# Kernel tuning notes

Measured on AMD Instinct MI355X. Metric: run time of the kernel, lower is better.

## Reference

```python
import jax, jax.numpy as jnp
import numpy as np

VOCAB, EMB, HID, LAYERS, SEQ, BATCH = 128, 512, 1024, 2, 256, 64


def _lstm_layer(xs, h0, c0, Wih, Whh, b):
    # xs: [S, B, in], h0/c0: [B, H], Wih: [4H, in], Whh: [4H, H], b: [4H]
    def step(carry, x_t):
        h, c = carry
        gates = x_t @ Wih.T + h @ Whh.T + b  # [B, 4H]
        i, f, g, o = jnp.split(gates, 4, axis=-1)
        c = jax.nn.sigmoid(f) * c + jax.nn.sigmoid(i) * jnp.tanh(g)
        h = jax.nn.sigmoid(o) * jnp.tanh(c)
        return (h, c), h

    (h, c), ys = jax.lax.scan(step, (h0, c0), xs)
    return ys, h, c


def setup_inputs() -> dict:
    key = jax.random.key(0)
    ks = jax.random.split(key, 10)
    s = 0.05
    inp = {
        "x": jax.random.randint(ks[0], (SEQ, BATCH), 0, VOCAB),
        "h0": jnp.zeros((LAYERS, BATCH, HID), jnp.float32),
        "c0": jnp.zeros((LAYERS, BATCH, HID), jnp.float32),
        "emb": jax.random.normal(ks[1], (VOCAB, EMB), jnp.float32) * s,
        "Wih0": jax.random.normal(ks[2], (4 * HID, EMB), jnp.float32) * s,
        "Whh0": jax.random.normal(ks[3], (4 * HID, HID), jnp.float32) * s,
        "b0": jnp.zeros((4 * HID,), jnp.float32),
        "Wih1": jax.random.normal(ks[4], (4 * HID, HID), jnp.float32) * s,
        "Whh1": jax.random.normal(ks[5], (4 * HID, HID), jnp.float32) * s,
        "b1": jnp.zeros((4 * HID,), jnp.float32),
        "Wfc": jax.random.normal(ks[6], (VOCAB, HID), jnp.float32) * s,
        "bfc": jnp.zeros((VOCAB,), jnp.float32),
    }
    return inp


def reference(x, h0, c0, emb, Wih0, Whh0, b0, Wih1, Whh1, b1, Wfc, bfc):
    xs = emb[x]  # [S, B, EMB] embedding lookup
    ys0, h_0, c_0 = _lstm_layer(xs, h0[0], c0[0], Wih0, Whh0, b0)
    ys1, h_1, c_1 = _lstm_layer(ys0, h0[1], c0[1], Wih1, Whh1, b1)
    last = ys1[-1]  # [B, HID]
    logits = last @ Wfc.T + bfc  # [B, VOCAB]
    hidden = (jnp.stack([h_0, h_1]), jnp.stack([c_0, c_1]))
    return (logits, hidden)
```

## Files before the change

### kernel.cpp

```cpp
#include <hip/hip_runtime.h>
#include <hip/hip_bf16.h>

#define SEQ   256
#define BATCH 64
#define HID   1024
#define EMBD  512
#define VOCAB 128
#define G4    4096
#define HBS   (BATCH * HID)

typedef short bf16x8_t __attribute__((ext_vector_type(8)));
typedef float f32x4_t  __attribute__((ext_vector_type(4)));
using bf16 = __hip_bfloat16;

__device__ __forceinline__ float sigm(float v) { return 1.f / (1.f + expf(-v)); }

__device__ __forceinline__ void cstore4(void* p, unsigned d) {
    asm volatile("global_store_dword %0, %1, off sc0 sc1" :: "v"(p), "v"(d) : "memory");
}

__global__ void cast_f32_bf16(const float* __restrict__ src, bf16* __restrict__ dst, int n) {
    int i = blockIdx.x * blockDim.x + threadIdx.x;
    int stride = gridDim.x * blockDim.x;
    for (; i < n; i += stride) dst[i] = __float2bfloat16(src[i]);
}

__global__ void init_all(const float* __restrict__ h0,
                         bf16* __restrict__ r0, bf16* __restrict__ r1,
                         unsigned* __restrict__ flags) {
    int i = blockIdx.x * blockDim.x + threadIdx.x;
    if (i < 512) flags[i] = 0u;
    int stride = gridDim.x * blockDim.x;
    for (int k = i; k < HBS; k += stride) {
        r0[k] = __float2bfloat16(h0[k]);
        r1[k] = __float2bfloat16(h0[HBS + k]);
    }
}

__global__ __launch_bounds__(256) void emb_gemm(
    const bf16* __restrict__ emb_bf, const bf16* __restrict__ Wih0_bf,
    const float* __restrict__ b0, float* __restrict__ E) {
    __shared__ float pb[4 * 128 * 17];
    const int tid = threadIdx.x, l = tid & 63, w = tid >> 6;
    const int lm = l & 15, k8 = (l >> 4) << 3;
    const int colbase = blockIdx.x * 16;
    const int gcol = colbase + lm;
    const int kq = w * 128;

    f32x4_t acc[8];
    #pragma unroll
    for (int rt = 0; rt < 8; ++rt) acc[rt] = f32x4_t{0.f, 0.f, 0.f, 0.f};
    bf16x8_t bf[4];
    #pragma unroll
    for (int k = 0; k < 4; ++k)
        bf[k] = *reinterpret_cast<const bf16x8_t*>(Wih0_bf + gcol * EMBD + kq + k * 32 + k8);
    #pragma unroll
    for (int k = 0; k < 4; ++k)
        #pragma unroll
        for (int rt = 0; rt < 8; ++rt) {
            bf16x8_t a = *reinterpret_cast<const bf16x8_t*>(
                emb_bf + (rt * 16 + lm) * EMBD + kq + k * 32 + k8);
            acc[rt] = __builtin_amdgcn_mfma_f32_16x16x32_bf16(a, bf[k], acc[rt], 0, 0, 0);
        }
    const int r0 = (l >> 4) << 2;
    #pragma unroll
    for (int rt = 0; rt < 8; ++rt)
        #pragma unroll
        for (int r = 0; r < 4; ++r)
            pb[(w * 128 + rt * 16 + r0 + r) * 17 + lm] = acc[rt][r];
    __syncthreads();
    #pragma unroll
    for (int i = 0; i < 8; ++i) {
        int p = tid + i * 256;
        int m = p >> 4, cc = p & 15;
        float g = pb[(0 * 128 + m) * 17 + cc] + pb[(1 * 128 + m) * 17 + cc]
                + pb[(2 * 128 + m) * 17 + cc] + pb[(3 * 128 + m) * 17 + cc];
        E[m * G4 + colbase + cc] = g + b0[colbase + cc];
    }
}

__device__ __forceinline__ void stage_slice(const char* slotB, char* Aregion,
                                            int kByte, int l) {
    #pragma unroll
    for (int i = 0; i < 32; ++i) {
        const int ci  = i * 64 + l;
        const int row = ci >> 5, kb = ci & 31;
        const char* g = slotB + row * 2048 + kByte + ((kb ^ (row & 7)) << 4);
        __builtin_amdgcn_global_load_lds(
            (const __attribute__((address_space(1))) unsigned*)g,
            (__attribute__((address_space(3))) unsigned*)(Aregion + i * 1024),
            16, 0, 0);
    }
}

__device__ __forceinline__ void issue_w(bf16x8_t (&bw)[2][8], const bf16* W,
                                        int gcol0, int gcol1, int kg, int lk) {
    #pragma unroll
    for (int nt = 0; nt < 2; ++nt) {
        const bf16* wb = W + (size_t)(nt == 0 ? gcol0 : gcol1) * HID + kg * 256 + lk * 8;
        #pragma unroll
        for (int kc = 0; kc < 8; ++kc)
            bw[nt][kc] = *reinterpret_cast<const bf16x8_t*>(wb + kc * 32);
    }
}

__device__ __forceinline__ void gemm_compute(const char* Aregion,
                                             const bf16x8_t (&bw)[2][8],
                                             int lm, int lk, f32x4_t (&acc)[4][2]) {
    asm volatile("s_waitcnt vmcnt(0)" ::: "memory");
    __builtin_amdgcn_sched_barrier(0);
    #pragma unroll
    for (int kc = 0; kc < 8; ++kc) {
        bf16x8_t a[4];
        #pragma unroll
        for (int mt = 0; mt < 4; ++mt) {
            const int row = mt * 16 + lm;
            a[mt] = *reinterpret_cast<const bf16x8_t*>(
                Aregion + row * 512 + ((kc * 64 + lk * 16) ^ ((row & 7) << 4)));
        }
        #pragma unroll
        for (int mt = 0; mt < 4; ++mt) {
            acc[mt][0] = __builtin_amdgcn_mfma_f32_16x16x32_bf16(a[mt], bw[0][kc], acc[mt][0], 0, 0, 0);
            acc[mt][1] = __builtin_amdgcn_mfma_f32_16x16x32_bf16(a[mt], bw[1][kc], acc[mt][1], 0, 0, 0);
        }
    }
}

__device__ __forceinline__ void pollslice(const unsigned* fbase, int kg,
                                          unsigned target, int l) {
    const unsigned* fp = fbase + kg * 32 + (l & 31);
    bool ok = (__hip_atomic_load(fp, __ATOMIC_RELAXED,
                                 __HIP_MEMORY_SCOPE_AGENT) >= target);
    while (!__all((int)ok)) {
        __builtin_amdgcn_s_sleep(1);
        ok = (__hip_atomic_load(fp, __ATOMIC_RELAXED,
                                __HIP_MEMORY_SCOPE_AGENT) >= target);
    }
}

template<int GRP>
__device__ __forceinline__ void run_layer(
    const int* __restrict__ x,
    const bf16* __restrict__ Wx, const bf16* __restrict__ Wh,
    const float* __restrict__ E, const float* __restrict__ b1,
    const float* __restrict__ c0,
    bf16* __restrict__ rSelf, const bf16* __restrict__ rOther,
    unsigned* __restrict__ flags, float* __restrict__ out,
    char* __restrict__ Abuf, float* __restrict__ pbuf, int tid, int wg)
{
    const int gl = wg & 127;
    const int hb = gl * 8;
    const int l  = tid & 63, kg = tid >> 6;
    const int lm = l & 15, lk = l >> 4;
    char* Areg = Abuf + kg * 32768;
    const int kByte = kg * 512;

    const int gcol0 = (0 + (lm >> 3)) * HID + hb + (lm & 7);
    const int gcol1 = (2 + (lm >> 3)) * HID + hb + (lm & 7);

    const int am = tid >> 2, cp = tid & 3;
    const int cc0 = cp * 2, col0 = hb + cc0;
    float creg[2];
    creg[0] = c0[GRP * HBS + am * HID + col0];
    creg[1] = c0[GRP * HBS + am * HID + col0 + 1];

    const unsigned* fA = flags;
    const unsigned* fOwn = flags + GRP * 128;
    unsigned* fMine = (unsigned*)(fOwn + gl);

    const int s_begin = (GRP == 0) ? 0 : 1;
    const int s_end   = (GRP == 0) ? SEQ : SEQ + 1;

    f32x4_t acc[4][2];
    auto zacc = [&]() {
        #pragma unroll
        for (int mt = 0; mt < 4; ++mt) {
            acc[mt][0] = f32x4_t{0.f, 0.f, 0.f, 0.f};
            acc[mt][1] = f32x4_t{0.f, 0.f, 0.f, 0.f};
        }
    };

    if (GRP == 1) {
        zacc();
        bf16x8_t bwx[2][8];
        issue_w(bwx, Wx, gcol0, gcol1, kg, lk);
        pollslice(fA, kg, 1u, l);
        stage_slice((const char*)(rOther + (size_t)1 * HBS), Areg, kByte, l);
        gemm_compute(Areg, bwx, lm, lk, acc);
        asm volatile("s_waitcnt lgkmcnt(0)" ::: "memory");
        __builtin_amdgcn_sched_barrier(0);
    }

    for (int s = s_begin; s < s_end; ++s) {
        float ep[4][2];
        if (GRP == 0) {
            const int xv = x[s * BATCH + am];
            const float* Ep = E + (size_t)xv * G4 + col0;
            #pragma unroll
            for (int sec = 0; sec < 4; ++sec) {
                ep[sec][0] = Ep[sec * HID];
                ep[sec][1] = Ep[sec * HID + 1];
            }
            zacc();
        }

        {
            bf16x8_t bw[2][8];
            issue_w(bw, Wh, gcol0, gcol1, kg, lk);
            if (GRP == 0) {
                pollslice(fOwn, kg, (unsigned)s, l);
                stage_slice((const char*)(rSelf + (size_t)s * HBS), Areg, kByte, l);
            } else {
                pollslice(fOwn, kg, (unsigned)(s - 1), l);
                stage_slice((const char*)(rSelf + (size_t)(s - 1) * HBS), Areg, kByte, l);
            }
            gemm_compute(Areg, bw, lm, lk, acc);
        }

        if (kg < 2) {
            #pragma unroll
            for (int mt = 0; mt < 4; ++mt)
                #pragma unroll
                for (int nt = 0; nt < 2; ++nt)
                    #pragma unroll
                    for (int r = 0; r < 4; ++r)
                        pbuf[(kg * 64 + mt * 16 + lk * 4 + r) * 34 + nt * 16 + lm]
                            = acc[mt][nt][r];
        }
        __syncthreads();
        if (kg >= 2) {
            #pragma unroll
            for (int mt = 0; mt < 4; ++mt)
                #pragma unroll
                for (int nt = 0; nt < 2; ++nt)
                    #pragma unroll
                    for (int r = 0; r < 4; ++r) {
                        float* p = &pbuf[((kg - 2) * 64 + mt * 16 + lk * 4 + r) * 34
                                         + nt * 16 + lm];
                        *p += acc[mt][nt][r];
                    }
        }
        __syncthreads();

        float g[4][2];
        #pragma unroll
        for (int sec = 0; sec < 4; ++sec) {
            const float* p0 = &pbuf[(0 * 64 + am) * 34 + sec * 8 + cc0];
            const float* p1 = &pbuf[(1 * 64 + am) * 34 + sec * 8 + cc0];
            g[sec][0] = p0[0] + p1[0];
            g[sec][1] = p0[1] + p1[1];
        }
        if (GRP == 0) {
            #pragma unroll
            for (int sec = 0; sec < 4; ++sec) {
                g[sec][0] += ep[sec][0];
                g[sec][1] += ep[sec][1];
            }
        } else {
            #pragma unroll
            for (int sec = 0; sec < 4; ++sec) {
                g[sec][0] += b1[sec * HID + col0];
                g[sec][1] += b1[sec * HID + col0 + 1];
            }
        }

        float hn[2];
        #pragma unroll
        for (int j = 0; j < 2; ++j) {
            float si = sigm(g[0][j]);
            float sf = sigm(g[1][j]);
            float tg = tanhf(g[2][j]);
            float so = sigm(g[3][j]);
            float cn = sf * creg[j] + si * tg;
            hn[j] = so * tanhf(cn);
            creg[j] = cn;
        }
        unsigned short u0 = __builtin_bit_cast(unsigned short, __float2bfloat16(hn[0]));
        unsigned short u1 = __builtin_bit_cast(unsigned short, __float2bfloat16(hn[1]));
        const int wslot = (GRP == 0) ? s + 1 : s;
        cstore4(rSelf + (size_t)wslot * HBS + am * HID + col0,
                (unsigned)u0 | ((unsigned)u1 << 16));

        const bool last = (GRP == 0) ? (s == SEQ - 1) : (s == SEQ);
        if (last) {
            float* oh = out + BATCH * VOCAB + GRP * HBS;
            float* oc = out + BATCH * VOCAB + 2 * HBS + GRP * HBS;
            oh[am * HID + col0]     = hn[0];
            oh[am * HID + col0 + 1] = hn[1];
            oc[am * HID + col0]     = creg[0];
            oc[am * HID + col0 + 1] = creg[1];
        }

        asm volatile("s_waitcnt vmcnt(0)" ::: "memory");
        __syncthreads();
        if (tid == 0) cstore4(fMine, (unsigned)wslot);

        if (GRP == 1 && s + 1 < s_end) {
            zacc();
            bf16x8_t bwx[2][8];
            issue_w(bwx, Wx, gcol0, gcol1, kg, lk);
            pollslice(fA, kg, (unsigned)(s + 1), l);
            stage_slice((const char*)(rOther + (size_t)(s + 1) * HBS), Areg, kByte, l);
            gemm_compute(Areg, bwx, lm, lk, acc);
            asm volatile("s_waitcnt lgkmcnt(0)" ::: "memory");
            __builtin_amdgcn_sched_barrier(0);
        }
    }
}

__global__ __launch_bounds__(256, 1) void lstm_persist(
    const int* __restrict__ x,
    const bf16* __restrict__ Whh0, const bf16* __restrict__ Wih1,
    const bf16* __restrict__ Whh1,
    const float* __restrict__ E, const float* __restrict__ b1,
    const float* __restrict__ c0,
    bf16* __restrict__ r0, bf16* __restrict__ r1,
    unsigned* __restrict__ flags, float* __restrict__ out)
{
    __shared__ char lds[131072 + 2 * 64 * 34 * 4];
    char*  Abuf = lds;
    float* pbuf = (float*)(lds + 131072);
    const int tid = threadIdx.x, wg = blockIdx.x;
    if (wg < 128)
        run_layer<0>(x, nullptr, Whh0, E, nullptr, c0, r0, nullptr, flags, out,
                     Abuf, pbuf, tid, wg);
    else
        run_layer<1>(x, Wih1, Whh1, E, b1, c0, r1, r0, flags, out,
                     Abuf, pbuf, tid, wg);
}

__global__ void logits_kernel(const float* __restrict__ h, const float* __restrict__ Wfc,
                              const float* __restrict__ bfc, float* __restrict__ out) {
    int t = blockIdx.x * blockDim.x + threadIdx.x;
    if (t >= BATCH * VOCAB) return;
    int m = t >> 7, v = t & 127;
    const float4* hp = reinterpret_cast<const float4*>(h + (size_t)m * HID);
    const float4* wp = reinterpret_cast<const float4*>(Wfc + (size_t)v * HID);
    float acc = 0.f;
    #pragma unroll 4
    for (int k = 0; k < HID / 4; ++k) {
        float4 a = hp[k], w = wp[k];
        acc += a.x * w.x + a.y * w.y + a.z * w.z + a.w * w.w;
    }
    out[t] = acc + bfc[v];
}

extern "C" void kernel_launch(void* const* d_in, const int* in_sizes, int n_in,
                              void* d_out, int out_size, void* d_ws, size_t ws_size,
                              hipStream_t stream) {
    const int*   x    = (const int*)d_in[0];
    const float* h0   = (const float*)d_in[1];
    const float* c0   = (const float*)d_in[2];
    const float* emb  = (const float*)d_in[3];
    const float* Wih0 = (const float*)d_in[4];
    const float* Whh0 = (const float*)d_in[5];
    const float* b0   = (const float*)d_in[6];
    const float* Wih1 = (const float*)d_in[7];
    const float* Whh1 = (const float*)d_in[8];
    const float* b1   = (const float*)d_in[9];
    const float* Wfc  = (const float*)d_in[10];
    const float* bfc  = (const float*)d_in[11];
    float* out = (float*)d_out;

    char* ws = (char*)d_ws;
    size_t off = 0;
    auto alloc = [&](size_t bytes) -> void* {
        void* p = ws + off;
        off += (bytes + 255) & ~(size_t)255;
        return p;
    };
    bf16*  Whh0_bf = (bf16*)alloc((size_t)G4 * HID * 2);
    bf16*  Wih1_bf = (bf16*)alloc((size_t)G4 * HID * 2);
    bf16*  Whh1_bf = (bf16*)alloc((size_t)G4 * HID * 2);
    float* E       = (float*)alloc((size_t)VOCAB * G4 * 4);
    bf16*  r0      = (bf16*)alloc((size_t)(SEQ + 1) * HBS * 2);
    bf16*  r1      = (bf16*)alloc((size_t)(SEQ + 1) * HBS * 2);
    unsigned* flags = (unsigned*)alloc(512 * 4);
    bf16* Wih0_bf  = (bf16*)alloc((size_t)G4 * EMBD * 2);
    bf16* emb_bf   = (bf16*)alloc((size_t)VOCAB * EMBD * 2);
    (void)ws_size; (void)in_sizes; (void)n_in; (void)out_size;

    cast_f32_bf16<<<64,  256, 0, stream>>>(emb,  emb_bf,  VOCAB * EMBD);
    cast_f32_bf16<<<512, 256, 0, stream>>>(Wih0, Wih0_bf, G4 * EMBD);
    cast_f32_bf16<<<512, 256, 0, stream>>>(Whh0, Whh0_bf, G4 * HID);
    cast_f32_bf16<<<512, 256, 0, stream>>>(Wih1, Wih1_bf, G4 * HID);
    cast_f32_bf16<<<512, 256, 0, stream>>>(Whh1, Whh1_bf, G4 * HID);
    init_all<<<64, 256, 0, stream>>>(h0, r0, r1, flags);
    emb_gemm<<<G4 / 16, 256, 0, stream>>>(emb_bf, Wih0_bf, b0, E);

    lstm_persist<<<256, 256, 0, stream>>>(x, Whh0_bf, Wih1_bf, Whh1_bf,
                                          E, b1, c0, r0, r1, flags, out);

    logits_kernel<<<(BATCH * VOCAB + 255) / 256, 256, 0, stream>>>(
        out + BATCH * VOCAB + HBS, Wfc, bfc, out);
}
```

Baseline: 1.900 ms.

## Keep LSTM weight slices resident in LDS with per-wave batch split and flags

Each persistent workgroup now loads its 32-column weight slice (both Wih1 and Whh1 for layer 1) into LDS once, instead of re-reading weights from global memory every timestep. Each wave now owns 16 batch rows over the full K dimension and reads the hidden-state rows directly into registers. This removes the cross-wave partial-sum reduction through LDS and the block-wide barriers. Synchronisation moves to per-wave flags, so each wave polls only the producers for its own batch rows. In exchange it uses many registers for A fragments and serialises the full-K MFMA chain within each wave.

```diff
diff --git a/kernel.cpp b/kernel.cpp
--- a/kernel.cpp
+++ b/kernel.cpp
@@ -15,6 +15,9 @@
 
 __device__ __forceinline__ float sigm(float v) { return 1.f / (1.f + expf(-v)); }
 
+__device__ __forceinline__ void cstore2(void* p, unsigned short d) {
+    asm volatile("global_store_short %0, %1, off sc0 sc1" :: "v"(p), "v"(d) : "memory");
+}
 __device__ __forceinline__ void cstore4(void* p, unsigned d) {
     asm volatile("global_store_dword %0, %1, off sc0 sc1" :: "v"(p), "v"(d) : "memory");
 }
@@ -29,7 +32,7 @@
                          bf16* __restrict__ r0, bf16* __restrict__ r1,
                          unsigned* __restrict__ flags) {
     int i = blockIdx.x * blockDim.x + threadIdx.x;
-    if (i < 512) flags[i] = 0u;
+    if (i < 1024) flags[i] = 0u;
     int stride = gridDim.x * blockDim.x;
     for (int k = i; k < HBS; k += stride) {
         r0[k] = __float2bfloat16(h0[k]);
@@ -79,62 +82,36 @@
     }
 }
 
-__device__ __forceinline__ void stage_slice(const char* slotB, char* Aregion,
-                                            int kByte, int l) {
-    #pragma unroll
-    for (int i = 0; i < 32; ++i) {
-        const int ci  = i * 64 + l;
-        const int row = ci >> 5, kb = ci & 31;
-        const char* g = slotB + row * 2048 + kByte + ((kb ^ (row & 7)) << 4);
-        __builtin_amdgcn_global_load_lds(
-            (const __attribute__((address_space(1))) unsigned*)g,
-            (__attribute__((address_space(3))) unsigned*)(Aregion + i * 1024),
-            16, 0, 0);
-    }
-}
-
-__device__ __forceinline__ void issue_w(bf16x8_t (&bw)[2][8], const bf16* W,
-                                        int gcol0, int gcol1, int kg, int lk) {
-    #pragma unroll
-    for (int nt = 0; nt < 2; ++nt) {
-        const bf16* wb = W + (size_t)(nt == 0 ? gcol0 : gcol1) * HID + kg * 256 + lk * 8;
-        #pragma unroll
-        for (int kc = 0; kc < 8; ++kc)
-            bw[nt][kc] = *reinterpret_cast<const bf16x8_t*>(wb + kc * 32);
-    }
-}
-
-__device__ __forceinline__ void gemm_compute(const char* Aregion,
-                                             const bf16x8_t (&bw)[2][8],
-                                             int lm, int lk, f32x4_t (&acc)[4][2]) {
+__device__ __forceinline__ void pollwave(const unsigned* fbase, unsigned target, int l) {
+    const unsigned* p0 = fbase + (l & 63);
+    const unsigned* p1 = fbase + 64 + (l & 63);
+    bool ok = (__hip_atomic_load(p0, __ATOMIC_RELAXED, __HIP_MEMORY_SCOPE_AGENT) >= target)
+           && (__hip_atomic_load(p1, __ATOMIC_RELAXED, __HIP_MEMORY_SCOPE_AGENT) >= target);
+    while (!__all((int)ok)) {
+        __builtin_amdgcn_s_sleep(1);
+        ok = (__hip_atomic_load(p0, __ATOMIC_RELAXED, __HIP_MEMORY_SCOPE_AGENT) >= target)
+          && (__hip_atomic_load(p1, __ATOMIC_RELAXED, __HIP_MEMORY_SCOPE_AGENT) >= target);
+    }
+}
+
+__device__ __forceinline__ void load_av(const bf16* arow, bf16x8_t (&av)[32]) {
+    #pragma unroll
+    for (int kc = 0; kc < 32; ++kc)
+        av[kc] = *reinterpret_cast<const bf16x8_t*>(arow + kc * 32);
     asm volatile("s_waitcnt vmcnt(0)" ::: "memory");
     __builtin_amdgcn_sched_barrier(0);
-    #pragma unroll
-    for (int kc = 0; kc < 8; ++kc) {
-        bf16x8_t a[4];
-        #pragma unroll
-        for (int mt = 0; mt < 4; ++mt) {
-            const int row = mt * 16 + lm;
-            a[mt] = *reinterpret_cast<const bf16x8_t*>(
-                Aregion + row * 512 + ((kc * 64 + lk * 16) ^ ((row & 7) << 4)));
-        }
-        #pragma unroll
-        for (int mt = 0; mt < 4; ++mt) {
-            acc[mt][0] = __builtin_amdgcn_mfma_f32_16x16x32_bf16(a[mt], bw[0][kc], acc[mt][0], 0, 0, 0);
-            acc[mt][1] = __builtin_amdgcn_mfma_f32_16x16x32_bf16(a[mt], bw[1][kc], acc[mt][1], 0, 0, 0);
-        }
-    }
-}
-
-__device__ __forceinline__ void pollslice(const unsigned* fbase, int kg,
-                                          unsigned target, int l) {
-    const unsigned* fp = fbase + kg * 32 + (l & 31);
-    bool ok = (__hip_atomic_load(fp, __ATOMIC_RELAXED,
-                                 __HIP_MEMORY_SCOPE_AGENT) >= target);
-    while (!__all((int)ok)) {
-        __builtin_amdgcn_s_sleep(1);
-        ok = (__hip_atomic_load(fp, __ATOMIC_RELAXED,
-                                __HIP_MEMORY_SCOPE_AGENT) >= target);
+}
+
+__device__ __forceinline__ void gemm_m16(const char* Wbase, const bf16x8_t (&av)[32],
+                                         int lm, int lk, f32x4_t (&acc)[2]) {
+    const int swz = (lm & 7) << 4;
+    #pragma unroll
+    for (int kc = 0; kc < 32; ++kc) {
+        const int kb = (kc * 64 + lk * 16) ^ swz;
+        bf16x8_t b0 = *reinterpret_cast<const bf16x8_t*>(Wbase + lm * 2048 + kb);
+        bf16x8_t b1 = *reinterpret_cast<const bf16x8_t*>(Wbase + (16 + lm) * 2048 + kb);
+        acc[0] = __builtin_amdgcn_mfma_f32_16x16x32_bf16(av[kc], b0, acc[0], 0, 0, 0);
+        acc[1] = __builtin_amdgcn_mfma_f32_16x16x32_bf16(av[kc], b1, acc[1], 0, 0, 0);
     }
 }
 
@@ -146,162 +123,139 @@
     const float* __restrict__ c0,
     bf16* __restrict__ rSelf, const bf16* __restrict__ rOther,
     unsigned* __restrict__ flags, float* __restrict__ out,
-    char* __restrict__ Abuf, float* __restrict__ pbuf, int tid, int wg)
+    char* __restrict__ Wlds, int tid, int wg)
 {
     const int gl = wg & 127;
     const int hb = gl * 8;
-    const int l  = tid & 63, kg = tid >> 6;
+    const int l  = tid & 63, w = tid >> 6;
     const int lm = l & 15, lk = l >> 4;
-    char* Areg = Abuf + kg * 32768;
-    const int kByte = kg * 512;
-
-    const int gcol0 = (0 + (lm >> 3)) * HID + hb + (lm & 7);
-    const int gcol1 = (2 + (lm >> 3)) * HID + hb + (lm & 7);
-
-    const int am = tid >> 2, cp = tid & 3;
-    const int cc0 = cp * 2, col0 = hb + cc0;
-    float creg[2];
-    creg[0] = c0[GRP * HBS + am * HID + col0];
-    creg[1] = c0[GRP * HBS + am * HID + col0 + 1];
-
-    const unsigned* fA = flags;
-    const unsigned* fOwn = flags + GRP * 128;
-    unsigned* fMine = (unsigned*)(fOwn + gl);
+
+    {
+        const bf16* wsrc0 = (GRP == 0) ? Wh : Wx;
+        #pragma unroll 4
+        for (int i = 0; i < 16; ++i) {
+            int chunk = tid + i * 256;
+            int row = chunk >> 7, cb = chunk & 127;
+            int gc = (row >> 3) * HID + hb + (row & 7);
+            bf16x8_t v = *reinterpret_cast<const bf16x8_t*>(wsrc0 + (size_t)gc * HID + cb * 8);
+            *reinterpret_cast<bf16x8_t*>(Wlds + row * 2048 + ((cb * 16) ^ ((row & 7) << 4))) = v;
+        }
+        if (GRP == 1) {
+            #pragma unroll 4
+            for (int i = 0; i < 16; ++i) {
+                int chunk = tid + i * 256;
+                int row = chunk >> 7, cb = chunk & 127;
+                int gc = (row >> 3) * HID + hb + (row & 7);
+                bf16x8_t v = *reinterpret_cast<const bf16x8_t*>(Wh + (size_t)gc * HID + cb * 8);
+                *reinterpret_cast<bf16x8_t*>(Wlds + 65536 + row * 2048 + ((cb * 16) ^ ((row & 7) << 4))) = v;
+            }
+        }
+    }
+    __syncthreads();
+
+    const char* Wx_lds = Wlds;
+    const char* Wh_lds = (GRP == 0) ? Wlds : (Wlds + 65536);
+
+    const int col = hb + (lm & 7);
+    const int mrow0 = w * 16 + lk * 4;
+    float creg[4];
+    if (lm < 8) {
+        #pragma unroll
+        for (int r = 0; r < 4; ++r)
+            creg[r] = c0[GRP * HBS + (size_t)(mrow0 + r) * HID + col];
+    }
+    float bias[4];
+    if (GRP == 1 && lm < 8) {
+        #pragma unroll
+        for (int sec = 0; sec < 4; ++sec) bias[sec] = b1[sec * HID + col];
+    }
+
+    const unsigned* fA   = flags + w * 128;
+    const unsigned* fOwn = flags + GRP * 512 + w * 128;
+    unsigned* fMine = (unsigned*)(flags + GRP * 512 + w * 128 + gl);
 
     const int s_begin = (GRP == 0) ? 0 : 1;
     const int s_end   = (GRP == 0) ? SEQ : SEQ + 1;
 
-    f32x4_t acc[4][2];
+    f32x4_t acc[2];
     auto zacc = [&]() {
-        #pragma unroll
-        for (int mt = 0; mt < 4; ++mt) {
-            acc[mt][0] = f32x4_t{0.f, 0.f, 0.f, 0.f};
-            acc[mt][1] = f32x4_t{0.f, 0.f, 0.f, 0.f};
-        }
+        acc[0] = f32x4_t{0.f, 0.f, 0.f, 0.f};
+        acc[1] = f32x4_t{0.f, 0.f, 0.f, 0.f};
     };
+
+    bf16x8_t av[32];
 
     if (GRP == 1) {
         zacc();
-        bf16x8_t bwx[2][8];
-        issue_w(bwx, Wx, gcol0, gcol1, kg, lk);
-        pollslice(fA, kg, 1u, l);
-        stage_slice((const char*)(rOther + (size_t)1 * HBS), Areg, kByte, l);
-        gemm_compute(Areg, bwx, lm, lk, acc);
+        pollwave(fA, 1u, l);
+        load_av(rOther + (size_t)1 * HBS + (size_t)(w * 16 + lm) * HID + lk * 8, av);
+        gemm_m16(Wx_lds, av, lm, lk, acc);
         asm volatile("s_waitcnt lgkmcnt(0)" ::: "memory");
         __builtin_amdgcn_sched_barrier(0);
     }
 
     for (int s = s_begin; s < s_end; ++s) {
-        float ep[4][2];
+        float ep[4][4];
         if (GRP == 0) {
-            const int xv = x[s * BATCH + am];
-            const float* Ep = E + (size_t)xv * G4 + col0;
+            zacc();
+            if (lm < 8) {
+                int xv[4];
+                #pragma unroll
+                for (int r = 0; r < 4; ++r) xv[r] = x[s * BATCH + mrow0 + r];
+                #pragma unroll
+                for (int r = 0; r < 4; ++r)
+                    #pragma unroll
+                    for (int sec = 0; sec < 4; ++sec)
+                        ep[sec][r] = E[(size_t)xv[r] * G4 + sec * HID + col];
+            }
+        }
+
+        if (GRP == 0) {
+            pollwave(fOwn, (unsigned)s, l);
+            load_av(rSelf + (size_t)s * HBS + (size_t)(w * 16 + lm) * HID + lk * 8, av);
+        } else {
+            pollwave(fOwn, (unsigned)(s - 1), l);
+            load_av(rSelf + (size_t)(s - 1) * HBS + (size_t)(w * 16 + lm) * HID + lk * 8, av);
+        }
+        gemm_m16(Wh_lds, av, lm, lk, acc);
+
+        float oth0[4], oth1[4];
+        #pragma unroll
+        for (int r = 0; r < 4; ++r) {
+            oth0[r] = __shfl_xor(acc[0][r], 8);
+            oth1[r] = __shfl_xor(acc[1][r], 8);
+        }
+        const int wslot = (GRP == 0) ? s + 1 : s;
+        if (lm < 8) {
+            bf16* rw = rSelf + (size_t)wslot * HBS;
+            const bool last = (GRP == 0) ? (s == SEQ - 1) : (s == SEQ);
             #pragma unroll
-            for (int sec = 0; sec < 4; ++sec) {
-                ep[sec][0] = Ep[sec * HID];
-                ep[sec][1] = Ep[sec * HID + 1];
+            for (int r = 0; r < 4; ++r) {
+                float vi = acc[0][r], vf = oth0[r], vg = acc[1][r], vo = oth1[r];
+                if (GRP == 0) { vi += ep[0][r]; vf += ep[1][r]; vg += ep[2][r]; vo += ep[3][r]; }
+                else          { vi += bias[0];  vf += bias[1];  vg += bias[2];  vo += bias[3]; }
+                float cn = sigm(vf) * creg[r] + sigm(vi) * tanhf(vg);
+                float hn = sigm(vo) * tanhf(cn);
+                creg[r] = cn;
+                unsigned short hu = __builtin_bit_cast(unsigned short, __float2bfloat16(hn));
+                cstore2(rw + (size_t)(mrow0 + r) * HID + col, hu);
+                if (last) {
+                    float* oh = out + BATCH * VOCAB + GRP * HBS;
+                    float* oc = out + BATCH * VOCAB + 2 * HBS + GRP * HBS;
+                    oh[(size_t)(mrow0 + r) * HID + col] = hn;
+                    oc[(size_t)(mrow0 + r) * HID + col] = cn;
+                }
             }
-            zacc();
-        }
-
-        {
-            bf16x8_t bw[2][8];
-            issue_w(bw, Wh, gcol0, gcol1, kg, lk);
-            if (GRP == 0) {
-                pollslice(fOwn, kg, (unsigned)s, l);
-                stage_slice((const char*)(rSelf + (size_t)s * HBS), Areg, kByte, l);
-            } else {
-                pollslice(fOwn, kg, (unsigned)(s - 1), l);
-                stage_slice((const char*)(rSelf + (size_t)(s - 1) * HBS), Areg, kByte, l);
-            }
-            gemm_compute(Areg, bw, lm, lk, acc);
-        }
-
-        if (kg < 2) {
-            #pragma unroll
-            for (int mt = 0; mt < 4; ++mt)
-                #pragma unroll
-                for (int nt = 0; nt < 2; ++nt)
-                    #pragma unroll
-                    for (int r = 0; r < 4; ++r)
-                        pbuf[(kg * 64 + mt * 16 + lk * 4 + r) * 34 + nt * 16 + lm]
-                            = acc[mt][nt][r];
-        }
-        __syncthreads();
-        if (kg >= 2) {
-            #pragma unroll
-            for (int mt = 0; mt < 4; ++mt)
-                #pragma unroll
-                for (int nt = 0; nt < 2; ++nt)
-                    #pragma unroll
-                    for (int r = 0; r < 4; ++r) {
-                        float* p = &pbuf[((kg - 2) * 64 + mt * 16 + lk * 4 + r) * 34
-                                         + nt * 16 + lm];
-                        *p += acc[mt][nt][r];
-                    }
-        }
-        __syncthreads();
-
-        float g[4][2];
-        #pragma unroll
-        for (int sec = 0; sec < 4; ++sec) {
-            const float* p0 = &pbuf[(0 * 64 + am) * 34 + sec * 8 + cc0];
-            const float* p1 = &pbuf[(1 * 64 + am) * 34 + sec * 8 + cc0];
-            g[sec][0] = p0[0] + p1[0];
-            g[sec][1] = p0[1] + p1[1];
-        }
-        if (GRP == 0) {
-            #pragma unroll
-            for (int sec = 0; sec < 4; ++sec) {
-                g[sec][0] += ep[sec][0];
-                g[sec][1] += ep[sec][1];
-            }
-        } else {
-            #pragma unroll
-            for (int sec = 0; sec < 4; ++sec) {
-                g[sec][0] += b1[sec * HID + col0];
-                g[sec][1] += b1[sec * HID + col0 + 1];
-            }
-        }
-
-        float hn[2];
-        #pragma unroll
-        for (int j = 0; j < 2; ++j) {
-            float si = sigm(g[0][j]);
-            float sf = sigm(g[1][j]);
-            float tg = tanhf(g[2][j]);
-            float so = sigm(g[3][j]);
-            float cn = sf * creg[j] + si * tg;
-            hn[j] = so * tanhf(cn);
-            creg[j] = cn;
-        }
-        unsigned short u0 = __builtin_bit_cast(unsigned short, __float2bfloat16(hn[0]));
-        unsigned short u1 = __builtin_bit_cast(unsigned short, __float2bfloat16(hn[1]));
-        const int wslot = (GRP == 0) ? s + 1 : s;
-        cstore4(rSelf + (size_t)wslot * HBS + am * HID + col0,
-                (unsigned)u0 | ((unsigned)u1 << 16));
-
-        const bool last = (GRP == 0) ? (s == SEQ - 1) : (s == SEQ);
-        if (last) {
-            float* oh = out + BATCH * VOCAB + GRP * HBS;
-            float* oc = out + BATCH * VOCAB + 2 * HBS + GRP * HBS;
-            oh[am * HID + col0]     = hn[0];
-            oh[am * HID + col0 + 1] = hn[1];
-            oc[am * HID + col0]     = creg[0];
-            oc[am * HID + col0 + 1] = creg[1];
         }
 
         asm volatile("s_waitcnt vmcnt(0)" ::: "memory");
-        __syncthreads();
-        if (tid == 0) cstore4(fMine, (unsigned)wslot);
+        if (l == 0) cstore4(fMine, (unsigned)wslot);
 
         if (GRP == 1 && s + 1 < s_end) {
             zacc();
-            bf16x8_t bwx[2][8];
-            issue_w(bwx, Wx, gcol0, gcol1, kg, lk);
-            pollslice(fA, kg, (unsigned)(s + 1), l);
-            stage_slice((const char*)(rOther + (size_t)(s + 1) * HBS), Areg, kByte, l);
-            gemm_compute(Areg, bwx, lm, lk, acc);
+            pollwave(fA, (unsigned)(s + 1), l);
+            load_av(rOther + (size_t)(s + 1) * HBS + (size_t)(w * 16 + lm) * HID + lk * 8, av);
+            gemm_m16(Wx_lds, av, lm, lk, acc);
             asm volatile("s_waitcnt lgkmcnt(0)" ::: "memory");
             __builtin_amdgcn_sched_barrier(0);
         }
@@ -317,16 +271,14 @@
     bf16* __restrict__ r0, bf16* __restrict__ r1,
     unsigned* __restrict__ flags, float* __restrict__ out)
 {
-    __shared__ char lds[131072 + 2 * 64 * 34 * 4];
-    char*  Abuf = lds;
-    float* pbuf = (float*)(lds + 131072);
+    __shared__ char Wlds[131072];
     const int tid = threadIdx.x, wg = blockIdx.x;
     if (wg < 128)
         run_layer<0>(x, nullptr, Whh0, E, nullptr, c0, r0, nullptr, flags, out,
-                     Abuf, pbuf, tid, wg);
+                     Wlds, tid, wg);
     else
         run_layer<1>(x, Wih1, Whh1, E, b1, c0, r1, r0, flags, out,
-                     Abuf, pbuf, tid, wg);
+                     Wlds, tid, wg);
 }
 
 __global__ void logits_kernel(const float* __restrict__ h, const float* __restrict__ Wfc,
@@ -375,7 +327,7 @@
     float* E       = (float*)alloc((size_t)VOCAB * G4 * 4);
     bf16*  r0      = (bf16*)alloc((size_t)(SEQ + 1) * HBS * 2);
     bf16*  r1      = (bf16*)alloc((size_t)(SEQ + 1) * HBS * 2);
-    unsigned* flags = (unsigned*)alloc(512 * 4);
+    unsigned* flags = (unsigned*)alloc(1024 * 4);
     bf16* Wih0_bf  = (bf16*)alloc((size_t)G4 * EMBD * 2);
     bf16* emb_bf   = (bf16*)alloc((size_t)VOCAB * EMBD * 2);
     (void)ws_size; (void)in_sizes; (void)n_in; (void)out_size;
```

Result: slower. 2.961 ms (+55.9%).
